# Performance work log

Hardware: AMD Instinct MI355X
Metric: run time of the kernel (lower is better)

The kernel has to match this reference:

```python
import jax, jax.numpy as jnp
import numpy as np

HIDDEN = 1024
HEADS = 16
HEAD_DIM = HIDDEN // HEADS
SCALE = HEAD_DIM ** -0.5
NEG_INF = -1e9  # finite stand-in for -inf so silu(masked) -> ~0 instead of NaN


def setup_inputs() -> dict:
    key = jax.random.key(0)
    ks = jax.random.split(key, 12)
    B, Sq, Sk = 2, 2048, 2048
    inp = {
        "query": jax.random.normal(ks[0], (B, Sq, HIDDEN), jnp.float32),
        "key": jax.random.normal(ks[1], (B, Sk, HIDDEN), jnp.float32),
        "value": jax.random.normal(ks[2], (B, Sk, HIDDEN), jnp.float32),
        "mask": jax.random.randint(ks[3], (B, 1, Sq, Sk), 0, 2, jnp.int32),
        # torch nn.Linear weights are [out_features, in_features]
        "Wq": jax.random.normal(ks[4], (HIDDEN, HIDDEN), jnp.float32) * 0.02,
        "bq": jax.random.normal(ks[5], (HIDDEN,), jnp.float32) * 0.02,
        "Wk": jax.random.normal(ks[6], (HIDDEN, HIDDEN), jnp.float32) * 0.02,
        "bk": jax.random.normal(ks[7], (HIDDEN,), jnp.float32) * 0.02,
        "Wv": jax.random.normal(ks[8], (HIDDEN, HIDDEN), jnp.float32) * 0.02,
        "bv": jax.random.normal(ks[9], (HIDDEN,), jnp.float32) * 0.02,
        "Wo": jax.random.normal(ks[10], (HIDDEN, HIDDEN), jnp.float32) * 0.02,
    }
    return inp


def _split_heads(x):
    B, S, _ = x.shape
    return x.reshape(B, S, HEADS, HEAD_DIM).transpose(0, 2, 1, 3)  # [B,H,S,D]


def reference(query, key, value, mask, Wq, bq, Wk, bk, Wv, bv, Wo):
    B, Sq, _ = query.shape
    q = _split_heads(query @ Wq.T + bq)   # [B,H,Sq,D]
    k = _split_heads(key @ Wk.T + bk)     # [B,H,Sk,D]
    v = _split_heads(value @ Wv.T + bv)   # [B,H,Sk,D]
    scores = jnp.einsum("bhqd,bhkd->bhqk", q, k) * SCALE
    scores = jnp.where(mask == 0, NEG_INF, scores)
    attn = jax.nn.silu(scores)            # silu in place of softmax (per source)
    # dropout is identity in eval mode
    out = jnp.einsum("bhqk,bhkd->bhqd", attn, v)
    out = out.transpose(0, 2, 1, 3).reshape(B, Sq, HIDDEN)
    return out @ Wo.T  # o_proj has no bias
```

## Files before the change

### kernel.cpp

```cpp
#include <hip/hip_runtime.h>
#include <hip/hip_bf16.h>

typedef __attribute__((ext_vector_type(4))) float f32x4;
typedef __attribute__((ext_vector_type(8))) short short8;

__device__ __forceinline__ unsigned short f2bf(float f) {
  unsigned int u = __float_as_uint(f);
  u += 0x7fffu + ((u >> 16) & 1u);
  return (unsigned short)(u >> 16);
}

__device__ __forceinline__ void g2lds16(const void* g, void* l) {
  __builtin_amdgcn_global_load_lds(
      (const __attribute__((address_space(1))) void*)g,
      (__attribute__((address_space(3))) void*)l, 16, 0, 0);
}

__global__ __launch_bounds__(256) void cvt_bf16(const float* __restrict__ src,
                                                unsigned short* __restrict__ dst,
                                                int n4) {
  int i = blockIdx.x * 256 + threadIdx.x;
  if (i >= n4) return;
  const float4 v = ((const float4*)src)[i];
  ushort4 o;
  o.x = f2bf(v.x); o.y = f2bf(v.y); o.z = f2bf(v.z); o.w = f2bf(v.w);
  ((ushort4*)dst)[i] = o;
}

__global__ __launch_bounds__(256) void pack_mask(const int* __restrict__ mask,
                                                 unsigned long long* __restrict__ mb) {
  int i = blockIdx.x * 256 + threadIdx.x;
  unsigned long long bits = __ballot(mask[i] != 0);
  if ((threadIdx.x & 63) == 0) mb[i >> 6] = bits;
}

template <int BIAS_MODE, int OUT_BF16>
__device__ __forceinline__ void gemm_tile(
    unsigned short* __restrict__ As, unsigned short* __restrict__ Bs,
    const unsigned short* __restrict__ A, const unsigned short* __restrict__ B,
    const float* __restrict__ bias, void* __restrict__ Cp,
    const int N, const int K, const int m0, const int n0, const float cscale) {
  const int tid  = (int)threadIdx.x;
  const int lane = tid & 63;
  const int wm   = tid >> 7;
  const int wn   = (tid >> 6) & 1;

  const f32x4 vzero = {0.f, 0.f, 0.f, 0.f};
  f32x4 acc[4][4];
#pragma unroll
  for (int mr = 0; mr < 4; ++mr)
#pragma unroll
    for (int nr = 0; nr < 4; ++nr) acc[mr][nr] = vzero;

  for (int k0 = 0; k0 < K; k0 += 64) {
#pragma unroll
    for (int i = 0; i < 4; ++i) {
      const int idx = i * 256 + tid;
      const int r = idx >> 3;
      const int c = idx & 7;
      const int koff = k0 + ((c ^ (r & 7)) << 3);
      g2lds16(A + (size_t)(m0 + r) * K + koff, &As[(i * 256 + (tid & 192)) * 8]);
      g2lds16(B + (size_t)(n0 + r) * K + koff, &Bs[(i * 256 + (tid & 192)) * 8]);
    }
    __syncthreads();
#pragma unroll
    for (int kk = 0; kk < 2; ++kk) {
      short8 af[4], bf[4];
#pragma unroll
      for (int mr = 0; mr < 4; ++mr) {
        const int row = wm * 64 + mr * 16 + (lane & 15);
        const int ch = (kk * 4 + (lane >> 4)) ^ (row & 7);
        af[mr] = *(const short8*)&As[row * 64 + ch * 8];
      }
#pragma unroll
      for (int nr = 0; nr < 4; ++nr) {
        const int row = wn * 64 + nr * 16 + (lane & 15);
        const int ch = (kk * 4 + (lane >> 4)) ^ (row & 7);
        bf[nr] = *(const short8*)&Bs[row * 64 + ch * 8];
      }
#pragma unroll
      for (int mr = 0; mr < 4; ++mr)
#pragma unroll
        for (int nr = 0; nr < 4; ++nr)
          acc[mr][nr] = __builtin_amdgcn_mfma_f32_16x16x32_bf16(af[mr], bf[nr],
                                                                acc[mr][nr], 0, 0, 0);
    }
    __syncthreads();
  }

#pragma unroll
  for (int mr = 0; mr < 4; ++mr) {
#pragma unroll
    for (int nr = 0; nr < 4; ++nr) {
#pragma unroll
      for (int rg = 0; rg < 4; ++rg) {
        const int row = m0 + wm * 64 + mr * 16 + ((lane >> 4) << 2) + rg;
        const int col = n0 + wn * 64 + nr * 16 + (lane & 15);
        float v = acc[mr][nr][rg];
        if (BIAS_MODE == 1) v += bias[col];
        if (BIAS_MODE == 2) v += bias[row];
        v *= cscale;
        if (OUT_BF16) ((unsigned short*)Cp)[(size_t)row * N + col] = f2bf(v);
        else          ((float*)Cp)[(size_t)row * N + col] = v;
      }
    }
  }
}

#define QSCALE 0.18033688011112042f
#define LN2    0.6931471805599453f

__global__ __launch_bounds__(256) void proj_qkv(
    const unsigned short* __restrict__ xq, const unsigned short* __restrict__ xk,
    const unsigned short* __restrict__ xv,
    const unsigned short* __restrict__ wq, const unsigned short* __restrict__ wk,
    const unsigned short* __restrict__ wv,
    const float* __restrict__ bq, const float* __restrict__ bk,
    const float* __restrict__ bv,
    unsigned short* __restrict__ qp, unsigned short* __restrict__ kp,
    unsigned short* __restrict__ vt) {
  __shared__ unsigned short As[128 * 64];
  __shared__ unsigned short Bs[128 * 64];
  const int z = blockIdx.z;
  if (z == 0) {
    gemm_tile<1, 1>(As, Bs, xq, wq, bq, qp, 1024, 1024, blockIdx.y * 128, blockIdx.x * 128, QSCALE);
  } else if (z == 1) {
    gemm_tile<1, 1>(As, Bs, xk, wk, bk, kp, 1024, 1024, blockIdx.y * 128, blockIdx.x * 128, 1.0f);
  } else {
    gemm_tile<2, 1>(As, Bs, wv, xv, bv, vt, 4096, 1024, blockIdx.x * 128, blockIdx.y * 128, 1.0f);
  }
}

__global__ __launch_bounds__(256) void out_proj(
    const unsigned short* __restrict__ ao, const unsigned short* __restrict__ wo,
    float* __restrict__ out) {
  __shared__ unsigned short As[128 * 64];
  __shared__ unsigned short Bs[128 * 64];
  gemm_tile<0, 0>(As, Bs, ao, wo, nullptr, out, 1024, 1024, blockIdx.y * 128, blockIdx.x * 128, 1.0f);
}

__global__ __launch_bounds__(256) void attn_kernel(
    const unsigned short* __restrict__ qp, const unsigned short* __restrict__ kp,
    const unsigned short* __restrict__ vt, const unsigned long long* __restrict__ mb,
    unsigned short* __restrict__ ao) {
  __shared__ unsigned short Ks[2][64 * 64];
  __shared__ unsigned short Vts[2][64 * 64];
  __shared__ unsigned short Ps[4 * 16 * 64];

  const int tid  = (int)threadIdx.x;
  const int lane = tid & 63;
  const int w    = tid >> 6;
  const int hi   = lane >> 4;
  const int c    = lane & 15;
  const int qbase = blockIdx.x * 64;
  const int h = blockIdx.y;
  const int b = blockIdx.z;
  const size_t tok0 = (size_t)b * 2048;

  const int qr = qbase + w * 16 + c;
  const unsigned short* qptr = qp + (tok0 + qr) * 1024 + h * 64 + (hi << 3);
  const short8 aq0 = *(const short8*)qptr;
  const short8 aq1 = *(const short8*)(qptr + 32);

  const unsigned long long* mql = mb + ((tok0 + qbase + w * 16 + hi * 4)) * 32;

  const f32x4 vzero = {0.f, 0.f, 0.f, 0.f};
  f32x4 oacc[4];
#pragma unroll
  for (int nr = 0; nr < 4; ++nr) oacc[nr] = vzero;

  const int sidx0 = tid;
  const int sidx1 = 256 + tid;

  {
#pragma unroll
    for (int i = 0; i < 2; ++i) {
      const int idx = i * 256 + tid;
      const int r = idx >> 3;
      const int cc = idx & 7;
      const int cs = (cc ^ (r & 7)) << 3;
      g2lds16(kp + (tok0 + r) * 1024 + h * 64 + cs, &Ks[0][(i * 256 + (tid & 192)) * 8]);
      g2lds16(vt + (size_t)(h * 64 + r) * 4096 + tok0 + cs, &Vts[0][(i * 256 + (tid & 192)) * 8]);
    }
  }
  __syncthreads();

  int buf = 0;
  for (int kt = 0; kt < 32; ++kt) {
    if (kt < 31) {
#pragma unroll
      for (int i = 0; i < 2; ++i) {
        const int idx = i * 256 + tid;
        const int r = idx >> 3;
        const int cc = idx & 7;
        const int cs = (cc ^ (r & 7)) << 3;
        g2lds16(kp + (tok0 + (kt + 1) * 64 + r) * 1024 + h * 64 + cs,
                &Ks[buf ^ 1][(i * 256 + (tid & 192)) * 8]);
        g2lds16(vt + (size_t)(h * 64 + r) * 4096 + tok0 + (kt + 1) * 64 + cs,
                &Vts[buf ^ 1][(i * 256 + (tid & 192)) * 8]);
      }
    }

    unsigned long long mrow[4];
#pragma unroll
    for (int rg = 0; rg < 4; ++rg) mrow[rg] = mql[rg * 32 + kt];

    f32x4 s[4];
    __builtin_amdgcn_s_setprio(1);
#pragma unroll
    for (int nr = 0; nr < 4; ++nr) {
      const int krow = nr * 16 + c;
      const short8 b0 = *(const short8*)&Ks[buf][krow * 64 + ((hi) ^ (krow & 7)) * 8];
      const short8 b1 = *(const short8*)&Ks[buf][krow * 64 + ((hi + 4) ^ (krow & 7)) * 8];
      f32x4 t = __builtin_amdgcn_mfma_f32_16x16x32_bf16(aq0, b0, vzero, 0, 0, 0);
      t = __builtin_amdgcn_mfma_f32_16x16x32_bf16(aq1, b1, t, 0, 0, 0);
      s[nr] = t;
    }
    __builtin_amdgcn_s_setprio(0);

#pragma unroll
    for (int rg = 0; rg < 4; ++rg) {
      const int row16 = (hi << 2) + rg;
      const unsigned long long ms = mrow[rg] >> c;
#pragma unroll
      for (int nr = 0; nr < 4; ++nr) {
        float sv = s[nr][rg];
        sv = ((unsigned int)(ms >> (nr * 16)) & 1u) ? sv : 0.f;
        const float p = sv * __builtin_amdgcn_rcpf(1.f + __builtin_amdgcn_exp2f(-sv));
        const unsigned int u = __float_as_uint(p) + 0x8000u;
        const int col = nr * 16 + c;
        Ps[w * 1024 + row16 * 64 + (((col >> 3) ^ (row16 & 7)) << 3) + (col & 7)] =
            (unsigned short)(u >> 16);
      }
    }

    const short8 pa0 = *(const short8*)&Ps[w * 1024 + c * 64 + ((hi) ^ (c & 7)) * 8];
    const short8 pa1 = *(const short8*)&Ps[w * 1024 + c * 64 + ((hi + 4) ^ (c & 7)) * 8];
    __builtin_amdgcn_s_setprio(1);
#pragma unroll
    for (int nr = 0; nr < 4; ++nr) {
      const int drow = nr * 16 + c;
      const short8 v0 = *(const short8*)&Vts[buf][drow * 64 + ((hi) ^ (drow & 7)) * 8];
      const short8 v1 = *(const short8*)&Vts[buf][drow * 64 + ((hi + 4) ^ (drow & 7)) * 8];
      oacc[nr] = __builtin_amdgcn_mfma_f32_16x16x32_bf16(pa0, v0, oacc[nr], 0, 0, 0);
      oacc[nr] = __builtin_amdgcn_mfma_f32_16x16x32_bf16(pa1, v1, oacc[nr], 0, 0, 0);
    }
    __builtin_amdgcn_s_setprio(0);

    __syncthreads();
    buf ^= 1;
  }

#pragma unroll
  for (int nr = 0; nr < 4; ++nr) {
#pragma unroll
    for (int rg = 0; rg < 4; ++rg) {
      const int row = qbase + w * 16 + (hi << 2) + rg;
      const int col = h * 64 + nr * 16 + c;
      ao[(tok0 + row) * 1024 + col] = f2bf(oacc[nr][rg] * LN2);
    }
  }
}

extern "C" void kernel_launch(void* const* d_in, const int* in_sizes, int n_in,
                              void* d_out, int out_size, void* d_ws, size_t ws_size,
                              hipStream_t stream) {
  (void)in_sizes; (void)n_in; (void)out_size; (void)ws_size;
  const float* query = (const float*)d_in[0];
  const float* key   = (const float*)d_in[1];
  const float* value = (const float*)d_in[2];
  const int*   mask  = (const int*)d_in[3];
  const float* Wq = (const float*)d_in[4];
  const float* bq = (const float*)d_in[5];
  const float* Wk = (const float*)d_in[6];
  const float* bk = (const float*)d_in[7];
  const float* Wv = (const float*)d_in[8];
  const float* bv = (const float*)d_in[9];
  const float* Wo = (const float*)d_in[10];

  char* ws = (char*)d_ws;
  const size_t MB = 1024 * 1024;
  unsigned short* xq  = (unsigned short*)(ws + 0 * MB);
  unsigned short* xk  = (unsigned short*)(ws + 8 * MB);
  unsigned short* xv  = (unsigned short*)(ws + 16 * MB);
  unsigned short* wqb = (unsigned short*)(ws + 24 * MB);
  unsigned short* wkb = (unsigned short*)(ws + 26 * MB);
  unsigned short* wvb = (unsigned short*)(ws + 28 * MB);
  unsigned short* wob = (unsigned short*)(ws + 30 * MB);
  unsigned short* qp  = (unsigned short*)(ws + 32 * MB);
  unsigned short* kp  = (unsigned short*)(ws + 40 * MB);
  unsigned short* vt  = (unsigned short*)(ws + 48 * MB);
  unsigned long long* mbq = (unsigned long long*)(ws + 56 * MB);
  unsigned short* ao  = (unsigned short*)(ws + 0 * MB);

  cvt_bf16<<<4096, 256, 0, stream>>>(query, xq, 1048576);
  cvt_bf16<<<4096, 256, 0, stream>>>(key,   xk, 1048576);
  cvt_bf16<<<4096, 256, 0, stream>>>(value, xv, 1048576);
  cvt_bf16<<<1024, 256, 0, stream>>>(Wq, wqb, 262144);
  cvt_bf16<<<1024, 256, 0, stream>>>(Wk, wkb, 262144);
  cvt_bf16<<<1024, 256, 0, stream>>>(Wv, wvb, 262144);
  cvt_bf16<<<1024, 256, 0, stream>>>(Wo, wob, 262144);
  pack_mask<<<32768, 256, 0, stream>>>(mask, mbq);

  proj_qkv<<<dim3(8, 32, 3), 256, 0, stream>>>(xq, xk, xv, wqb, wkb, wvb,
                                               bq, bk, bv, qp, kp, vt);
  attn_kernel<<<dim3(32, 16, 2), 256, 0, stream>>>(qp, kp, vt, mbq, ao);
  out_proj<<<dim3(8, 32), 256, 0, stream>>>(ao, wob, (float*)d_out);
}
```

Before: 183.9 us.

## Rework attention to 32x32 MFMA with register-resident P and merged conversion kernels

The attention kernel now uses 2 waves of 32 query rows each and 32x32x16 bf16 MFMAs, computing S transposed (K as the A operand) so that the SiLU probabilities can be packed with v_cvt_pk_bf16_f32 and redistributed through v_permlane32_swap straight into the PV MFMA operand. This removes the per-tile LDS round-trip for P. Mask bits are applied with a bitfield-extract AND instead of a select. The seven separate fp32-to-bf16 conversion launches are merged into two launches to cut launch overhead. The risks are halved threads per block, which affects staging parallelism and occupancy, and correctness that depends on the exact MFMA lane layout.

```diff
diff --git a/kernel.cpp b/kernel.cpp
--- a/kernel.cpp
+++ b/kernel.cpp
@@ -2,7 +2,9 @@
 #include <hip/hip_bf16.h>
 
 typedef __attribute__((ext_vector_type(4))) float f32x4;
+typedef __attribute__((ext_vector_type(16))) float f32x16;
 typedef __attribute__((ext_vector_type(8))) short short8;
+typedef __attribute__((ext_vector_type(4))) unsigned int uint4v;
 
 __device__ __forceinline__ unsigned short f2bf(float f) {
   unsigned int u = __float_as_uint(f);
@@ -16,15 +18,36 @@
       (__attribute__((address_space(3))) void*)l, 16, 0, 0);
 }
 
-__global__ __launch_bounds__(256) void cvt_bf16(const float* __restrict__ src,
-                                                unsigned short* __restrict__ dst,
-                                                int n4) {
-  int i = blockIdx.x * 256 + threadIdx.x;
-  if (i >= n4) return;
-  const float4 v = ((const float4*)src)[i];
+__global__ __launch_bounds__(256) void cvt3(const float* __restrict__ s0,
+                                            const float* __restrict__ s1,
+                                            const float* __restrict__ s2,
+                                            unsigned short* __restrict__ d0,
+                                            unsigned short* __restrict__ d1,
+                                            unsigned short* __restrict__ d2) {
+  const int i = blockIdx.x * 256 + threadIdx.x;
+  const float* s = blockIdx.y == 0 ? s0 : (blockIdx.y == 1 ? s1 : s2);
+  unsigned short* d = blockIdx.y == 0 ? d0 : (blockIdx.y == 1 ? d1 : d2);
+  const float4 v = ((const float4*)s)[i];
   ushort4 o;
   o.x = f2bf(v.x); o.y = f2bf(v.y); o.z = f2bf(v.z); o.w = f2bf(v.w);
-  ((ushort4*)dst)[i] = o;
+  ((ushort4*)d)[i] = o;
+}
+
+__global__ __launch_bounds__(256) void cvt4(const float* __restrict__ s0,
+                                            const float* __restrict__ s1,
+                                            const float* __restrict__ s2,
+                                            const float* __restrict__ s3,
+                                            unsigned short* __restrict__ d0,
+                                            unsigned short* __restrict__ d1,
+                                            unsigned short* __restrict__ d2,
+                                            unsigned short* __restrict__ d3) {
+  const int i = blockIdx.x * 256 + threadIdx.x;
+  const float* s = blockIdx.y == 0 ? s0 : (blockIdx.y == 1 ? s1 : (blockIdx.y == 2 ? s2 : s3));
+  unsigned short* d = blockIdx.y == 0 ? d0 : (blockIdx.y == 1 ? d1 : (blockIdx.y == 2 ? d2 : d3));
+  const float4 v = ((const float4*)s)[i];
+  ushort4 o;
+  o.x = f2bf(v.x); o.y = f2bf(v.y); o.z = f2bf(v.z); o.w = f2bf(v.w);
+  ((ushort4*)d)[i] = o;
 }
 
 __global__ __launch_bounds__(256) void pack_mask(const int* __restrict__ mask,
@@ -139,125 +162,119 @@
   gemm_tile<0, 0>(As, Bs, ao, wo, nullptr, out, 1024, 1024, blockIdx.y * 128, blockIdx.x * 128, 1.0f);
 }
 
-__global__ __launch_bounds__(256) void attn_kernel(
+__global__ __launch_bounds__(128, 2) void attn_kernel(
     const unsigned short* __restrict__ qp, const unsigned short* __restrict__ kp,
     const unsigned short* __restrict__ vt, const unsigned long long* __restrict__ mb,
     unsigned short* __restrict__ ao) {
   __shared__ unsigned short Ks[2][64 * 64];
   __shared__ unsigned short Vts[2][64 * 64];
-  __shared__ unsigned short Ps[4 * 16 * 64];
 
   const int tid  = (int)threadIdx.x;
   const int lane = tid & 63;
   const int w    = tid >> 6;
-  const int hi   = lane >> 4;
-  const int c    = lane & 15;
+  const int c32  = lane & 31;
+  const int lo   = lane >> 5;
   const int qbase = blockIdx.x * 64;
   const int h = blockIdx.y;
-  const int b = blockIdx.z;
-  const size_t tok0 = (size_t)b * 2048;
-
-  const int qr = qbase + w * 16 + c;
-  const unsigned short* qptr = qp + (tok0 + qr) * 1024 + h * 64 + (hi << 3);
-  const short8 aq0 = *(const short8*)qptr;
-  const short8 aq1 = *(const short8*)(qptr + 32);
-
-  const unsigned long long* mql = mb + ((tok0 + qbase + w * 16 + hi * 4)) * 32;
-
-  const f32x4 vzero = {0.f, 0.f, 0.f, 0.f};
-  f32x4 oacc[4];
-#pragma unroll
-  for (int nr = 0; nr < 4; ++nr) oacc[nr] = vzero;
-
-  const int sidx0 = tid;
-  const int sidx1 = 256 + tid;
-
-  {
-#pragma unroll
-    for (int i = 0; i < 2; ++i) {
-      const int idx = i * 256 + tid;
+  const size_t tok0 = (size_t)blockIdx.z * 2048;
+
+  const int q = qbase + w * 32 + c32;
+  const unsigned short* qptr = qp + (tok0 + q) * 1024 + h * 64 + lo * 8;
+  short8 qf[4];
+#pragma unroll
+  for (int kd = 0; kd < 4; ++kd) qf[kd] = *(const short8*)(qptr + kd * 16);
+
+  const unsigned long long* mql = mb + (tok0 + q) * 32;
+
+  f32x16 oacc[2];
+#pragma unroll
+  for (int dt = 0; dt < 2; ++dt)
+#pragma unroll
+    for (int r = 0; r < 16; ++r) oacc[dt][r] = 0.f;
+
+  auto stage = [&](int kt_, int bf_) {
+#pragma unroll
+    for (int i = 0; i < 4; ++i) {
+      const int idx = i * 128 + tid;
       const int r = idx >> 3;
       const int cc = idx & 7;
       const int cs = (cc ^ (r & 7)) << 3;
-      g2lds16(kp + (tok0 + r) * 1024 + h * 64 + cs, &Ks[0][(i * 256 + (tid & 192)) * 8]);
-      g2lds16(vt + (size_t)(h * 64 + r) * 4096 + tok0 + cs, &Vts[0][(i * 256 + (tid & 192)) * 8]);
-    }
-  }
+      g2lds16(kp + (tok0 + kt_ * 64 + r) * 1024 + h * 64 + cs,
+              &Ks[bf_][(i * 128 + (tid & 64)) * 8]);
+      g2lds16(vt + (size_t)(h * 64 + r) * 4096 + tok0 + kt_ * 64 + cs,
+              &Vts[bf_][(i * 128 + (tid & 64)) * 8]);
+    }
+  };
+
+  stage(0, 0);
   __syncthreads();
 
+  const f32x16 z16 = {0.f};
   int buf = 0;
   for (int kt = 0; kt < 32; ++kt) {
-    if (kt < 31) {
-#pragma unroll
-      for (int i = 0; i < 2; ++i) {
-        const int idx = i * 256 + tid;
-        const int r = idx >> 3;
-        const int cc = idx & 7;
-        const int cs = (cc ^ (r & 7)) << 3;
-        g2lds16(kp + (tok0 + (kt + 1) * 64 + r) * 1024 + h * 64 + cs,
-                &Ks[buf ^ 1][(i * 256 + (tid & 192)) * 8]);
-        g2lds16(vt + (size_t)(h * 64 + r) * 4096 + tok0 + (kt + 1) * 64 + cs,
-                &Vts[buf ^ 1][(i * 256 + (tid & 192)) * 8]);
-      }
-    }
-
-    unsigned long long mrow[4];
-#pragma unroll
-    for (int rg = 0; rg < 4; ++rg) mrow[rg] = mql[rg * 32 + kt];
-
-    f32x4 s[4];
-    __builtin_amdgcn_s_setprio(1);
-#pragma unroll
-    for (int nr = 0; nr < 4; ++nr) {
-      const int krow = nr * 16 + c;
-      const short8 b0 = *(const short8*)&Ks[buf][krow * 64 + ((hi) ^ (krow & 7)) * 8];
-      const short8 b1 = *(const short8*)&Ks[buf][krow * 64 + ((hi + 4) ^ (krow & 7)) * 8];
-      f32x4 t = __builtin_amdgcn_mfma_f32_16x16x32_bf16(aq0, b0, vzero, 0, 0, 0);
-      t = __builtin_amdgcn_mfma_f32_16x16x32_bf16(aq1, b1, t, 0, 0, 0);
-      s[nr] = t;
-    }
-    __builtin_amdgcn_s_setprio(0);
-
-#pragma unroll
-    for (int rg = 0; rg < 4; ++rg) {
-      const int row16 = (hi << 2) + rg;
-      const unsigned long long ms = mrow[rg] >> c;
-#pragma unroll
-      for (int nr = 0; nr < 4; ++nr) {
-        float sv = s[nr][rg];
-        sv = ((unsigned int)(ms >> (nr * 16)) & 1u) ? sv : 0.f;
-        const float p = sv * __builtin_amdgcn_rcpf(1.f + __builtin_amdgcn_exp2f(-sv));
-        const unsigned int u = __float_as_uint(p) + 0x8000u;
-        const int col = nr * 16 + c;
-        Ps[w * 1024 + row16 * 64 + (((col >> 3) ^ (row16 & 7)) << 3) + (col & 7)] =
-            (unsigned short)(u >> 16);
-      }
-    }
-
-    const short8 pa0 = *(const short8*)&Ps[w * 1024 + c * 64 + ((hi) ^ (c & 7)) * 8];
-    const short8 pa1 = *(const short8*)&Ps[w * 1024 + c * 64 + ((hi + 4) ^ (c & 7)) * 8];
-    __builtin_amdgcn_s_setprio(1);
-#pragma unroll
-    for (int nr = 0; nr < 4; ++nr) {
-      const int drow = nr * 16 + c;
-      const short8 v0 = *(const short8*)&Vts[buf][drow * 64 + ((hi) ^ (drow & 7)) * 8];
-      const short8 v1 = *(const short8*)&Vts[buf][drow * 64 + ((hi + 4) ^ (drow & 7)) * 8];
-      oacc[nr] = __builtin_amdgcn_mfma_f32_16x16x32_bf16(pa0, v0, oacc[nr], 0, 0, 0);
-      oacc[nr] = __builtin_amdgcn_mfma_f32_16x16x32_bf16(pa1, v1, oacc[nr], 0, 0, 0);
-    }
-    __builtin_amdgcn_s_setprio(0);
+    if (kt < 31) stage(kt + 1, buf ^ 1);
+    const unsigned long long m = mql[kt];
+
+#pragma unroll
+    for (int t = 0; t < 2; ++t) {
+      f32x16 st = z16;
+      __builtin_amdgcn_s_setprio(1);
+#pragma unroll
+      for (int kd = 0; kd < 4; ++kd) {
+        const int krt = t * 32 + c32;
+        const short8 kf = *(const short8*)&Ks[buf][krt * 64 + (((2 * kd + lo) ^ (c32 & 7)) << 3)];
+        st = __builtin_amdgcn_mfma_f32_32x32x16_bf16(kf, qf[kd], st, 0, 0, 0);
+      }
+      __builtin_amdgcn_s_setprio(0);
+
+      const unsigned int ms = (unsigned int)(m >> (t * 32 + lo * 4));
+      float pv[16];
+#pragma unroll
+      for (int r = 0; r < 16; ++r) {
+        const int krow = (r & 3) + 8 * (r >> 2);
+        const int smear = __builtin_amdgcn_sbfe((int)ms, krow, 1);
+        const float sv = __int_as_float(__float_as_int(st[r]) & smear);
+        pv[r] = sv * __builtin_amdgcn_rcpf(1.f + __builtin_amdgcn_exp2f(-sv));
+      }
+
+      unsigned int u[8];
+#pragma unroll
+      for (int g = 0; g < 4; ++g) {
+        asm("v_cvt_pk_bf16_f32 %0, %1, %2" : "=v"(u[2 * g])     : "v"(pv[4 * g]),     "v"(pv[4 * g + 1]));
+        asm("v_cvt_pk_bf16_f32 %0, %1, %2" : "=v"(u[2 * g + 1]) : "v"(pv[4 * g + 2]), "v"(pv[4 * g + 3]));
+      }
+      asm("v_permlane32_swap_b32 %0, %1" : "+v"(u[0]), "+v"(u[2]));
+      asm("v_permlane32_swap_b32 %0, %1" : "+v"(u[1]), "+v"(u[3]));
+      asm("v_permlane32_swap_b32 %0, %1" : "+v"(u[4]), "+v"(u[6]));
+      asm("v_permlane32_swap_b32 %0, %1" : "+v"(u[5]), "+v"(u[7]));
+      const uint4v wA = {u[0], u[1], u[2], u[3]};
+      const uint4v wB = {u[4], u[5], u[6], u[7]};
+      const short8 paA = __builtin_bit_cast(short8, wA);
+      const short8 paB = __builtin_bit_cast(short8, wB);
+
+      __builtin_amdgcn_s_setprio(1);
+#pragma unroll
+      for (int dt = 0; dt < 2; ++dt) {
+        const int drow = dt * 32 + c32;
+        const short8 vf0 = *(const short8*)&Vts[buf][drow * 64 + (((4 * t + lo) ^ (c32 & 7)) << 3)];
+        const short8 vf1 = *(const short8*)&Vts[buf][drow * 64 + (((4 * t + 2 + lo) ^ (c32 & 7)) << 3)];
+        oacc[dt] = __builtin_amdgcn_mfma_f32_32x32x16_bf16(paA, vf0, oacc[dt], 0, 0, 0);
+        oacc[dt] = __builtin_amdgcn_mfma_f32_32x32x16_bf16(paB, vf1, oacc[dt], 0, 0, 0);
+      }
+      __builtin_amdgcn_s_setprio(0);
+    }
 
     __syncthreads();
     buf ^= 1;
   }
 
 #pragma unroll
-  for (int nr = 0; nr < 4; ++nr) {
-#pragma unroll
-    for (int rg = 0; rg < 4; ++rg) {
-      const int row = qbase + w * 16 + (hi << 2) + rg;
-      const int col = h * 64 + nr * 16 + c;
-      ao[(tok0 + row) * 1024 + col] = f2bf(oacc[nr][rg] * LN2);
+  for (int dt = 0; dt < 2; ++dt) {
+#pragma unroll
+    for (int r = 0; r < 16; ++r) {
+      const int row = qbase + w * 32 + (r & 3) + 8 * (r >> 2) + 4 * lo;
+      const int col = h * 64 + dt * 32 + c32;
+      ao[(tok0 + row) * 1024 + col] = f2bf(oacc[dt][r] * LN2);
     }
   }
 }
@@ -293,17 +310,12 @@
   unsigned long long* mbq = (unsigned long long*)(ws + 56 * MB);
   unsigned short* ao  = (unsigned short*)(ws + 0 * MB);
 
-  cvt_bf16<<<4096, 256, 0, stream>>>(query, xq, 1048576);
-  cvt_bf16<<<4096, 256, 0, stream>>>(key,   xk, 1048576);
-  cvt_bf16<<<4096, 256, 0, stream>>>(value, xv, 1048576);
-  cvt_bf16<<<1024, 256, 0, stream>>>(Wq, wqb, 262144);
-  cvt_bf16<<<1024, 256, 0, stream>>>(Wk, wkb, 262144);
-  cvt_bf16<<<1024, 256, 0, stream>>>(Wv, wvb, 262144);
-  cvt_bf16<<<1024, 256, 0, stream>>>(Wo, wob, 262144);
+  cvt3<<<dim3(4096, 3), 256, 0, stream>>>(query, key, value, xq, xk, xv);
+  cvt4<<<dim3(1024, 4), 256, 0, stream>>>(Wq, Wk, Wv, Wo, wqb, wkb, wvb, wob);
   pack_mask<<<32768, 256, 0, stream>>>(mask, mbq);
 
   proj_qkv<<<dim3(8, 32, 3), 256, 0, stream>>>(xq, xk, xv, wqb, wkb, wvb,
                                                bq, bk, bv, qp, kp, vt);
-  attn_kernel<<<dim3(32, 16, 2), 256, 0, stream>>>(qp, kp, vt, mbq, ao);
+  attn_kernel<<<dim3(32, 16, 2), 128, 0, stream>>>(qp, kp, vt, mbq, ao);
   out_proj<<<dim3(8, 32), 256, 0, stream>>>(ao, wob, (float*)d_out);
 }
```

Measured after the change: 199.0 us. 1.08x slower.
